# Optimization experiments

Measured on AMD Instinct MI355X. Metric: run time of the kernel, lower is better.

## Reference

```python
import jax, jax.numpy as jnp
import numpy as np

N = 8192
HID = 256
NCLS = 5
K = 10  # adj_parameter
IN_DIMS = [1000, 1000, 503]


def _leaky(x):
    return jnp.where(x >= 0, x, 0.25 * x)


def _batchnorm(x, g, b):
    # training-mode BatchNorm1d with batch stats (biased var), eps=1e-5
    mu = jnp.mean(x, axis=0)
    var = jnp.mean((x - mu) ** 2, axis=0)
    return (x - mu) * jax.lax.rsqrt(var + 1e-5) * g + b


def _build_adj(feat):
    # cosine similarity, per-row top-(K+1) (top-1 is self, diag=1), scatter,
    # add identity, L1 row-normalize. Vectorized equivalent of the torch loop.
    norm = jnp.maximum(jnp.linalg.norm(feat, axis=1, keepdims=True), 1e-12)
    fn = feat / norm
    sim = fn @ fn.T                                  # [N, N]
    vals, idx = jax.lax.top_k(sim, K + 1)            # [N, K+1]
    rows = jnp.arange(sim.shape[0])[:, None]
    adj = jnp.zeros_like(sim).at[rows, idx[:, 1:]].set(vals[:, 1:])
    adj = adj + jnp.eye(sim.shape[0], dtype=sim.dtype)
    rs = jnp.maximum(jnp.sum(jnp.abs(adj), axis=1, keepdims=True), 1e-12)
    return adj / rs


def setup_inputs() -> dict:
    key = jax.random.key(0)
    ks = jax.random.split(key, 24)
    d = {}
    d['x1'] = jax.random.normal(ks[0], (N, IN_DIMS[0]), jnp.float32)
    d['x2'] = jax.random.normal(ks[1], (N, IN_DIMS[1]), jnp.float32)
    d['x3'] = jax.random.normal(ks[2], (N, IN_DIMS[2]), jnp.float32)
    def xavier(k, shape):
        fan_in, fan_out = shape[-2], shape[-1]
        std = np.sqrt(2.0 / (fan_in + fan_out))
        return jax.random.normal(k, shape, jnp.float32) * std
    d['enc_W1'] = xavier(ks[3], (IN_DIMS[0], HID))
    d['enc_W2'] = xavier(ks[4], (IN_DIMS[1], HID))
    d['enc_W3'] = xavier(ks[5], (IN_DIMS[2], HID))
    d['enc_b'] = jnp.zeros((3, HID), jnp.float32)
    d['bn_g'] = jnp.ones((3, HID), jnp.float32)
    d['bn_b'] = jnp.zeros((3, HID), jnp.float32)
    d['gc1_W'] = xavier(ks[6], (3, HID, HID))
    d['gc1_b'] = jnp.zeros((3, HID), jnp.float32)
    d['gc2_W'] = xavier(ks[7], (3, HID, HID))
    d['gc2_b'] = jnp.zeros((3, HID), jnp.float32)
    d['clf_W'] = xavier(ks[8], (3, HID, NCLS))
    d['clf_b'] = jnp.zeros((3, NCLS), jnp.float32)
    d['attn'] = xavier(ks[9], (3, 1))[:, 0]
    d['f1_W'] = xavier(ks[10], (NCLS, 128))
    d['f1_b'] = jnp.zeros((128,), jnp.float32)
    d['f2_W'] = xavier(ks[11], (128, NCLS))
    d['f2_b'] = jnp.zeros((NCLS,), jnp.float32)
    return d


def reference(x1, x2, x3, enc_W1, enc_W2, enc_W3, enc_b, bn_g, bn_b,
              gc1_W, gc1_b, gc2_W, gc2_b, clf_W, clf_b,
              attn, f1_W, f1_b, f2_W, f2_b):
    xs = [x1, x2, x3]
    enc_Ws = [enc_W1, enc_W2, enc_W3]
    logits_list = []
    for i in range(3):
        # modal encoder: Linear -> ReLU -> BatchNorm (dropout off, eval)
        feat = jax.nn.relu(xs[i] @ enc_Ws[i] + enc_b[i])
        feat = _batchnorm(feat, bn_g[i], bn_b[i])
        adj = _build_adj(feat)
        # SimpleGCN: two GraphConvolution layers with leaky_relu(0.25)
        h = _leaky(adj @ (feat @ gc1_W[i]) + gc1_b[i])
        h = _leaky(adj @ (h @ gc2_W[i]) + gc2_b[i])
        logits_list.append(h @ clf_W[i] + clf_b[i])
    # SimpleVCDN fusion
    w = jax.nn.softmax(attn)
    fused = sum(w[i] * jax.nn.sigmoid(logits_list[i]) for i in range(3))
    out = _leaky(fused @ f1_W + f1_b) @ f2_W + f2_b
    return out
```

## Files before the change

### kernel.cpp

```cpp
#include <hip/hip_runtime.h>
#include <cfloat>
#include <cstdint>
#include <cstddef>

#define NROWS 8192
#define HID 256
#define NCLS 5
#define TOPK 10
#define CAP 256
#define TM 128
#define TN 128
#define BK 32
#define BKS 64

typedef __bf16 bf16x8 __attribute__((ext_vector_type(8)));
typedef float f32x4 __attribute__((ext_vector_type(4)));

__device__ inline ushort f2bf(float x) {
  unsigned u = __float_as_uint(x);
  unsigned r = (u + 0x7fffu + ((u >> 16) & 1u)) >> 16;
  return (ushort)r;
}
__device__ inline float bf2f(ushort b) { return __uint_as_float(((unsigned)b) << 16); }

__device__ __forceinline__ void load_lds16(const void* g, void* l) {
  __builtin_amdgcn_global_load_lds(
      (const __attribute__((address_space(1))) void*)g,
      (__attribute__((address_space(3))) void*)l, 16, 0, 0);
}

__global__ __launch_bounds__(256) void packAB_kernel(const float* __restrict__ X0,
    const float* __restrict__ X1, const float* __restrict__ X2,
    const float* __restrict__ W0, const float* __restrict__ W1,
    const float* __restrict__ W2, ushort* __restrict__ Ah, ushort* __restrict__ Al,
    ushort* __restrict__ Bh, ushort* __restrict__ Bl,
    int D0, int D1, int D2, int Kp0, int Kp1, int Kp2,
    size_t aOff0, size_t aOff1, size_t aOff2,
    size_t wOff0, size_t wOff1, size_t wOff2) {
  const int z = blockIdx.y;
  const float* X = (z == 0) ? X0 : (z == 1) ? X1 : X2;
  const float* W = (z == 0) ? W0 : (z == 1) ? W1 : W2;
  const int D = (z == 0) ? D0 : (z == 1) ? D1 : D2;
  const int Kp = (z == 0) ? Kp0 : (z == 1) ? Kp1 : Kp2;
  const size_t aOff = (z == 0) ? aOff0 : (z == 1) ? aOff1 : aOff2;
  const size_t wOff = (z == 0) ? wOff0 : (z == 1) ? wOff1 : wOff2;
  const int ksh = 31 - __clz(Kp);
  const int id = blockIdx.x * 256 + threadIdx.x;
  const int atotal = NROWS << ksh;
  if (id >= atotal + (HID << ksh)) return;
  if (id < atotal) {
    const int k = id & (Kp - 1);
    const int r = id >> ksh;
    const float x = (k < D) ? X[(size_t)r * D + k] : 0.f;
    const ushort h = f2bf(x);
    Ah[aOff + id] = h;
    Al[aOff + id] = f2bf(x - bf2f(h));
  } else {
    const int id2 = id - atotal;
    const int k = id2 & (Kp - 1);
    const int n = id2 >> ksh;
    const float x = (k < D) ? W[(size_t)k * HID + n] : 0.f;
    const ushort h = f2bf(x);
    Bh[wOff + id2] = h;
    Bl[wOff + id2] = f2bf(x - bf2f(h));
  }
}

__global__ __launch_bounds__(256) void packW_kernel(const float* __restrict__ W,
    ushort* __restrict__ Bh, ushort* __restrict__ Bl) {
  const int z = blockIdx.y;
  const int id = blockIdx.x * 256 + threadIdx.x;
  const int k = id >> 8, n = id & 255;
  const size_t wz = (size_t)z * HID * HID;
  const float x = W[wz + (size_t)k * HID + n];
  const ushort h = f2bf(x);
  Bh[wz + (size_t)n * HID + k] = h;
  Bl[wz + (size_t)n * HID + k] = f2bf(x - bf2f(h));
}

template<bool BIAS, int ACT>
__global__ __launch_bounds__(256) void limbgemm_kernel(const ushort* __restrict__ Ah,
    const ushort* __restrict__ Al, const ushort* __restrict__ Bh,
    const ushort* __restrict__ Bl, const float* __restrict__ bias,
    float* __restrict__ C, int Kp0, int Kp1, int Kp2,
    size_t aOff0, size_t aOff1, size_t aOff2,
    size_t bOff0, size_t bOff1, size_t bOff2) {
  __shared__ ushort AsH[64 * BK], AsL[64 * BK], BsH[64 * BK], BsL[64 * BK];
  const int z = blockIdx.y;
  const int Kp = (z == 0) ? Kp0 : (z == 1) ? Kp1 : Kp2;
  const size_t aO = (z == 0) ? aOff0 : (z == 1) ? aOff1 : aOff2;
  const size_t bO = (z == 0) ? bOff0 : (z == 1) ? bOff1 : bOff2;
  Ah += aO; Al += aO; Bh += bO; Bl += bO;
  C += (size_t)z * NROWS * HID;
  const int tid = threadIdx.x;
  const int wave = tid >> 6, lane = tid & 63;
  const int bid = blockIdx.x;
  const int xcd = bid & 7, slot = bid >> 3;
  const int bxi = slot & 3;
  const int byi = xcd * 16 + (slot >> 2);
  const int bm = byi * 64, bn = bxi * 64;
  const int wr = (wave >> 1) * 32, wc = (wave & 1) * 32;

  f32x4 acc[2][2];
  const f32x4 zero = {0.f, 0.f, 0.f, 0.f};
  acc[0][0] = zero; acc[0][1] = zero; acc[1][0] = zero; acc[1][1] = zero;

  const int r0 = tid >> 2, kl0 = (tid & 3) ^ ((r0 & 3) ^ ((r0 >> 2) & 1));
  const size_t aoff = (size_t)(bm + r0) * Kp + kl0 * 8;
  const size_t boff = (size_t)(bn + r0) * Kp + kl0 * 8;

  for (int k0 = 0; k0 < Kp; k0 += BK) {
    __syncthreads();
    load_lds16(Ah + aoff + k0, &AsH[tid * 8]);
    load_lds16(Al + aoff + k0, &AsL[tid * 8]);
    load_lds16(Bh + boff + k0, &BsH[tid * 8]);
    load_lds16(Bl + boff + k0, &BsL[tid * 8]);
    __syncthreads();
    bf16x8 ah[2], al[2], bh[2], bl[2];
    const int kg = lane >> 4;
    #pragma unroll
    for (int f = 0; f < 2; ++f) {
      const int m = wr + f * 16 + (lane & 15);
      const int sa = m * 4 + (kg ^ (m & 3) ^ ((m >> 2) & 1));
      ah[f] = *(const bf16x8*)&AsH[sa * 8];
      al[f] = *(const bf16x8*)&AsL[sa * 8];
      const int n = wc + f * 16 + (lane & 15);
      const int sb = n * 4 + (kg ^ (n & 3) ^ ((n >> 2) & 1));
      bh[f] = *(const bf16x8*)&BsH[sb * 8];
      bl[f] = *(const bf16x8*)&BsL[sb * 8];
    }
    #pragma unroll
    for (int fr = 0; fr < 2; ++fr)
      #pragma unroll
      for (int fc = 0; fc < 2; ++fc) {
        acc[fr][fc] = __builtin_amdgcn_mfma_f32_16x16x32_bf16(ah[fr], bh[fc], acc[fr][fc], 0, 0, 0);
        acc[fr][fc] = __builtin_amdgcn_mfma_f32_16x16x32_bf16(ah[fr], bl[fc], acc[fr][fc], 0, 0, 0);
        acc[fr][fc] = __builtin_amdgcn_mfma_f32_16x16x32_bf16(al[fr], bh[fc], acc[fr][fc], 0, 0, 0);
      }
  }
  const int cq = lane >> 4, cc = lane & 15;
  #pragma unroll
  for (int fr = 0; fr < 2; ++fr) {
    #pragma unroll
    for (int fc = 0; fc < 2; ++fc) {
      const int rb = bm + wr + fr * 16 + cq * 4;
      const int col = bn + wc + fc * 16 + cc;
      const float bb = BIAS ? bias[z * HID + col] : 0.f;
      float* cp = C + (size_t)rb * HID + col;
      #pragma unroll
      for (int e = 0; e < 4; ++e) {
        float v = acc[fr][fc][e] + bb;
        if (ACT == 1) v = fmaxf(v, 0.f);
        cp[(size_t)e * HID] = v;
      }
    }
  }
}

__global__ __launch_bounds__(256) void bn_stats_kernel(const float* __restrict__ F,
    float* __restrict__ ps, float* __restrict__ ps2) {
  const int z = blockIdx.y;
  const int b = blockIdx.x, t = threadIdx.x;
  float s = 0.f, s2 = 0.f;
  const float* p = F + (size_t)z * NROWS * HID + (size_t)b * 128 * HID + t;
  for (int r = 0; r < 128; ++r) {
    const float v = p[(size_t)r * HID];
    s += v; s2 += v * v;
  }
  ps[(size_t)z * 64 * HID + b * HID + t] = s;
  ps2[(size_t)z * 64 * HID + b * HID + t] = s2;
}

__global__ __launch_bounds__(256) void bn_finalize_kernel(const float* __restrict__ ps,
    const float* __restrict__ ps2, const float* __restrict__ g,
    const float* __restrict__ b, float* __restrict__ scale, float* __restrict__ shift) {
  const int z = blockIdx.x;
  const int t = threadIdx.x;
  float s = 0.f, s2 = 0.f;
  for (int i = 0; i < 64; ++i) {
    s += ps[(size_t)z * 64 * HID + i * HID + t];
    s2 += ps2[(size_t)z * 64 * HID + i * HID + t];
  }
  const float mu = s / (float)NROWS;
  const float var = s2 / (float)NROWS - mu * mu;
  const float rstd = rsqrtf(var + 1e-5f);
  const float sc = rstd * g[z * HID + t];
  scale[z * HID + t] = sc;
  shift[z * HID + t] = b[z * HID + t] - mu * sc;
}

__global__ __launch_bounds__(256) void bn_rownorm_kernel(const float* __restrict__ F,
    const float* __restrict__ scale, const float* __restrict__ shift,
    float* __restrict__ FN, ushort* __restrict__ Ph,
    ushort* __restrict__ Fh, ushort* __restrict__ Fl) {
  const int z = blockIdx.y;
  const int r = blockIdx.x, t = threadIdx.x;
  const size_t zb = (size_t)z * NROWS * HID;
  const float f = F[zb + (size_t)r * HID + t] * scale[z * HID + t] + shift[z * HID + t];
  __shared__ float sh[256];
  sh[t] = f * f;
  __syncthreads();
  for (int st = 128; st > 0; st >>= 1) {
    if (t < st) sh[t] += sh[t + st];
    __syncthreads();
  }
  const float inv = 1.0f / fmaxf(sqrtf(sh[0]), 1e-12f);
  const float fn = f * inv;
  const size_t o = zb + (size_t)r * HID + t;
  FN[o] = fn;
  Ph[o] = f2bf(fn);
  const ushort h = f2bf(f);
  Fh[o] = h;
  Fl[o] = f2bf(f - bf2f(h));
}

template<int PASS>
__global__ __launch_bounds__(512) void simtile_kernel(const ushort* __restrict__ P,
    float* __restrict__ M, const float* __restrict__ tauv,
    int* __restrict__ gcnt, int* __restrict__ gidx) {
  const int bx = blockIdx.x, by = blockIdx.y;
  if (by > bx) return;
  const int z = blockIdx.z;
  P += (size_t)z * NROWS * HID;
  if (PASS == 0) M += (size_t)z * NROWS * 64;
  else {
    tauv += (size_t)z * NROWS;
    gcnt += (size_t)z * NROWS;
    gidx += (size_t)z * NROWS * CAP;
  }
  const bool offdiag = (bx != by);
  __shared__ ushort As[TM * BKS];
  __shared__ ushort Bs[TN * BKS];
  __shared__ float Ml[2][TM];
  __shared__ float MlC[4][TN];
  __shared__ float taulA[TM];
  __shared__ float taulB[TN];
  const int tid = threadIdx.x;
  const int wave = tid >> 6, lane = tid & 63;
  const int bm = by * TM;
  const int bn = bx * TN;
  const int wr = (wave >> 1) * 32;
  const int wc = (wave & 1) * 64;

  if (PASS == 1) {
    if (tid < TM) taulA[tid] = tauv[bm + tid];
    else if (tid < TM + TN) taulB[tid - TM] = tauv[bn + (tid - TM)];
  }

  const ushort* pa[2];
  const ushort* pb[2];
  #pragma unroll
  for (int j = 0; j < 2; ++j) {
    const int s = tid + j * 512;
    const int m = s >> 3;
    const int kg = (s & 7) ^ (m & 7);
    pa[j] = P + (size_t)(bm + m) * HID + kg * 8;
    pb[j] = P + (size_t)(bn + m) * HID + kg * 8;
  }

  f32x4 acc[2][4];
  const f32x4 zero = {0.f, 0.f, 0.f, 0.f};
  #pragma unroll
  for (int i = 0; i < 2; ++i)
    #pragma unroll
    for (int j = 0; j < 4; ++j) acc[i][j] = zero;

  for (int k0 = 0; k0 < HID; k0 += BKS) {
    __syncthreads();
    #pragma unroll
    for (int j = 0; j < 2; ++j) {
      load_lds16(pa[j] + k0, &As[(tid + j * 512) * 8]);
      load_lds16(pb[j] + k0, &Bs[(tid + j * 512) * 8]);
    }
    __syncthreads();
    #pragma unroll
    for (int h = 0; h < 2; ++h) {
      const int kgb = h * 4 + (lane >> 4);
      bf16x8 af[2], bf[4];
      #pragma unroll
      for (int f = 0; f < 2; ++f) {
        const int m = wr + f * 16 + (lane & 15);
        const int sa = m * 8 + (kgb ^ (m & 7));
        af[f] = *(const bf16x8*)&As[sa * 8];
      }
      #pragma unroll
      for (int f = 0; f < 4; ++f) {
        const int n = wc + f * 16 + (lane & 15);
        const int sb = n * 8 + (kgb ^ (n & 7));
        bf[f] = *(const bf16x8*)&Bs[sb * 8];
      }
      #pragma unroll
      for (int fr = 0; fr < 2; ++fr)
        #pragma unroll
        for (int fc = 0; fc < 4; ++fc)
          acc[fr][fc] = __builtin_amdgcn_mfma_f32_16x16x32_bf16(af[fr], bf[fc], acc[fr][fc], 0, 0, 0);
    }
  }

  const int cq = lane >> 4, cc = lane & 15;
  if (PASS == 0) {
    #pragma unroll
    for (int fr = 0; fr < 2; ++fr) {
      #pragma unroll
      for (int e = 0; e < 4; ++e) {
        const int lrow = wr + fr * 16 + cq * 4 + e;
        const int grow = bm + lrow;
        float mx = -FLT_MAX;
        #pragma unroll
        for (int fc = 0; fc < 4; ++fc) {
          const int col = bn + wc + fc * 16 + cc;
          mx = fmaxf(mx, (col == grow) ? -FLT_MAX : acc[fr][fc][e]);
        }
        #pragma unroll
        for (int s = 1; s < 16; s <<= 1) mx = fmaxf(mx, __shfl_xor(mx, s));
        if (cc == 0) Ml[wave & 1][lrow] = mx;
      }
    }
    if (offdiag) {
      #pragma unroll
      for (int fc = 0; fc < 4; ++fc) {
        float mx = -FLT_MAX;
        #pragma unroll
        for (int fr = 0; fr < 2; ++fr)
          #pragma unroll
          for (int e = 0; e < 4; ++e) mx = fmaxf(mx, acc[fr][fc][e]);
        mx = fmaxf(mx, __shfl_xor(mx, 16));
        mx = fmaxf(mx, __shfl_xor(mx, 32));
        if (cq == 0) MlC[wave >> 1][wc + fc * 16 + cc] = mx;
      }
    }
    __syncthreads();
    if (tid < TM) M[(size_t)(bm + tid) * 64 + bx] = fmaxf(Ml[0][tid], Ml[1][tid]);
    if (offdiag && tid < TN) {
      const float mx = fmaxf(fmaxf(MlC[0][tid], MlC[1][tid]),
                             fmaxf(MlC[2][tid], MlC[3][tid]));
      M[(size_t)(bn + tid) * 64 + by] = mx;
    }
  } else {
    __syncthreads();
    #pragma unroll
    for (int fr = 0; fr < 2; ++fr) {
      #pragma unroll
      for (int e = 0; e < 4; ++e) {
        const int lrow = wr + fr * 16 + cq * 4 + e;
        const int grow = bm + lrow;
        const float tA = taulA[lrow];
        #pragma unroll
        for (int fc = 0; fc < 4; ++fc) {
          const int lcol = wc + fc * 16 + cc;
          const int gcol = bn + lcol;
          const float v = acc[fr][fc][e];
          if (gcol != grow && v >= tA) {
            const int pos = atomicAdd(&gcnt[grow], 1);
            if (pos < CAP) gidx[(size_t)grow * CAP + pos] = gcol;
          }
          if (offdiag && v >= taulB[lcol]) {
            const int pos = atomicAdd(&gcnt[gcol], 1);
            if (pos < CAP) gidx[(size_t)gcol * CAP + pos] = grow;
          }
        }
      }
    }
  }
}

__global__ __launch_bounds__(256) void tau_kernel(const float* __restrict__ M,
    float* __restrict__ tauv, int* __restrict__ gcnt) {
  const int z = blockIdx.y;
  const int wave = threadIdx.x >> 6, lane = threadIdx.x & 63;
  const int row = blockIdx.x * 4 + wave;
  float cur = M[(size_t)z * NROWS * 64 + (size_t)row * 64 + lane];
  float tau = cur;
  #pragma unroll
  for (int sel = 0; sel < 16; ++sel) {
    float bv = cur;
    int bl = lane;
    #pragma unroll
    for (int s = 1; s < 64; s <<= 1) {
      const float ov = __shfl_xor(bv, s);
      const int ol = __shfl_xor(bl, s);
      if (ov > bv || (ov == bv && ol < bl)) { bv = ov; bl = ol; }
    }
    tau = bv;
    if (lane == bl) cur = -FLT_MAX;
  }
  if (lane == 0) {
    tauv[(size_t)z * NROWS + row] = tau;
    gcnt[(size_t)z * NROWS + row] = 0;
  }
}

__global__ __launch_bounds__(256) void refine_kernel(const int* __restrict__ gcnt,
    const int* __restrict__ gidx, const float* __restrict__ FN,
    int* __restrict__ nidx, float* __restrict__ nval, float* __restrict__ dinv) {
  const int z = blockIdx.y;
  gcnt += (size_t)z * NROWS;
  gidx += (size_t)z * NROWS * CAP;
  FN += (size_t)z * NROWS * HID;
  nidx += (size_t)z * NROWS * TOPK;
  nval += (size_t)z * NROWS * TOPK;
  dinv += (size_t)z * NROWS;
  const int wave = threadIdx.x >> 6, lane = threadIdx.x & 63;
  const int row = blockIdx.x * 4 + wave;
  const int cnt = min(gcnt[row], CAP);
  __shared__ float fnrow[4][HID];
  __shared__ float ev[4][CAP];
  ((float4*)fnrow[wave])[lane] = ((const float4*)(FN + (size_t)row * HID))[lane];
  __syncthreads();
  const int c = lane >> 2, q4 = lane & 3;
  for (int b0 = 0; b0 < cnt; b0 += 16) {
    const int ci = b0 + c;
    const int cand = (ci < cnt) ? gidx[(size_t)row * CAP + ci] : 0;
    float s = 0.f;
    const float* fc = FN + (size_t)cand * HID + q4 * 64;
    const float* fr = fnrow[wave] + q4 * 64;
    #pragma unroll 8
    for (int k = 0; k < 64; ++k) s += fr[k] * fc[k];
    s += __shfl_xor(s, 1);
    s += __shfl_xor(s, 2);
    if (q4 == 0 && ci < cnt) ev[wave][ci] = s;
  }
  __syncthreads();
  float outv[TOPK];
  int outi[TOPK];
  float sum = 1.0f;
  #pragma unroll
  for (int sel = 0; sel < TOPK; ++sel) {
    float bv = -FLT_MAX;
    int bp = 0;
    #pragma unroll
    for (int j = 0; j < 4; ++j) {
      const int p = lane + j * 64;
      if (p < cnt) {
        const float v = ev[wave][p];
        if (v > bv) { bv = v; bp = p; }
      }
    }
    #pragma unroll
    for (int s = 1; s < 64; s <<= 1) {
      const float ov = __shfl_xor(bv, s);
      const int op = __shfl_xor(bp, s);
      if (ov > bv || (ov == bv && op < bp)) { bv = ov; bp = op; }
    }
    outv[sel] = bv;
    outi[sel] = bp;
    sum += fabsf(bv);
    if (lane == 0) ev[wave][bp] = -FLT_MAX;
  }
  if (lane == 0) {
    const float inv = 1.0f / fmaxf(sum, 1e-12f);
    dinv[row] = inv;
    #pragma unroll
    for (int sel = 0; sel < TOPK; ++sel) {
      nval[row * TOPK + sel] = outv[sel] * inv;
      nidx[row * TOPK + sel] = gidx[(size_t)row * CAP + outi[sel]];
    }
  }
}

template<int EMIT>
__global__ __launch_bounds__(256) void spmm_kernel(const float* __restrict__ T,
    const int* __restrict__ nidx, const float* __restrict__ nval,
    const float* __restrict__ dinv, const float* __restrict__ bias,
    float* __restrict__ H, ushort* __restrict__ Hh, ushort* __restrict__ Hl) {
  const int z = blockIdx.y;
  const size_t zb = (size_t)z * NROWS * HID;
  T += zb;
  nidx += (size_t)z * NROWS * TOPK;
  nval += (size_t)z * NROWS * TOPK;
  dinv += (size_t)z * NROWS;
  const int r = blockIdx.x, c = threadIdx.x;
  float acc = dinv[r] * T[(size_t)r * HID + c];
  #pragma unroll
  for (int n = 0; n < TOPK; ++n) {
    acc += nval[r * TOPK + n] * T[(size_t)nidx[r * TOPK + n] * HID + c];
  }
  acc += bias[z * HID + c];
  const float v = acc >= 0.f ? acc : 0.25f * acc;
  const size_t o = zb + (size_t)r * HID + c;
  if (EMIT == 0) {
    H[o] = v;
  } else {
    const ushort h = f2bf(v);
    Hh[o] = h;
    Hl[o] = f2bf(v - bf2f(h));
  }
}

__global__ __launch_bounds__(256) void clf_kernel(const float* __restrict__ H,
    const float* __restrict__ W, const float* __restrict__ b,
    float* __restrict__ L) {
  const int z = blockIdx.y;
  const int id = blockIdx.x * 256 + threadIdx.x;
  if (id >= NROWS * NCLS) return;
  const int r = id / NCLS, c = id % NCLS;
  float s = b[z * NCLS + c];
  const float* hr = H + (size_t)z * NROWS * HID + (size_t)r * HID;
  const float* wz = W + (size_t)z * HID * NCLS;
  for (int k = 0; k < HID; ++k) s += hr[k] * wz[k * NCLS + c];
  L[(size_t)z * NROWS * NCLS + id] = s;
}

__global__ __launch_bounds__(256) void fuse_kernel(const float* __restrict__ L,
    const float* __restrict__ attn, float* __restrict__ fused) {
  const int id = blockIdx.x * 256 + threadIdx.x;
  if (id >= NROWS * NCLS) return;
  const float a0 = attn[0], a1 = attn[1], a2 = attn[2];
  const float m = fmaxf(a0, fmaxf(a1, a2));
  const float e0 = expf(a0 - m), e1 = expf(a1 - m), e2 = expf(a2 - m);
  const float inv = 1.0f / (e0 + e1 + e2);
  const float l0 = L[id];
  const float l1 = L[NROWS * NCLS + id];
  const float l2 = L[2 * NROWS * NCLS + id];
  const float s0 = 1.0f / (1.0f + expf(-l0));
  const float s1 = 1.0f / (1.0f + expf(-l1));
  const float s2 = 1.0f / (1.0f + expf(-l2));
  fused[id] = (e0 * s0 + e1 * s1 + e2 * s2) * inv;
}

__global__ __launch_bounds__(128) void head_kernel(const float* __restrict__ fused,
    const float* __restrict__ W1, const float* __restrict__ b1,
    const float* __restrict__ W2, const float* __restrict__ b2,
    float* __restrict__ out) {
  const int r = blockIdx.x, t = threadIdx.x;
  __shared__ float f[NCLS];
  __shared__ float hh[128];
  if (t < NCLS) f[t] = fused[r * NCLS + t];
  __syncthreads();
  float s = b1[t];
  #pragma unroll
  for (int k = 0; k < NCLS; ++k) s += f[k] * W1[k * 128 + t];
  hh[t] = s >= 0.f ? s : 0.25f * s;
  __syncthreads();
  if (t < NCLS) {
    float o = b2[t];
    for (int k = 0; k < 128; ++k) o += hh[k] * W2[k * NCLS + t];
    out[r * NCLS + t] = o;
  }
}

extern "C" void kernel_launch(void* const* d_in, const int* in_sizes, int n_in,
                              void* d_out, int out_size, void* d_ws, size_t ws_size,
                              hipStream_t stream) {
  const float* x0 = (const float*)d_in[0];
  const float* x1 = (const float*)d_in[1];
  const float* x2 = (const float*)d_in[2];
  const float* eW0 = (const float*)d_in[3];
  const float* eW1 = (const float*)d_in[4];
  const float* eW2 = (const float*)d_in[5];
  const float* enc_b = (const float*)d_in[6];
  const float* bn_g  = (const float*)d_in[7];
  const float* bn_b  = (const float*)d_in[8];
  const float* gc1W  = (const float*)d_in[9];
  const float* gc1b  = (const float*)d_in[10];
  const float* gc2W  = (const float*)d_in[11];
  const float* gc2b  = (const float*)d_in[12];
  const float* clfW  = (const float*)d_in[13];
  const float* clfb  = (const float*)d_in[14];
  const float* attn  = (const float*)d_in[15];
  const float* f1W   = (const float*)d_in[16];
  const float* f1b   = (const float*)d_in[17];
  const float* f2W   = (const float*)d_in[18];
  const float* f2b   = (const float*)d_in[19];
  float* out = (float*)d_out;

  int Kp[3];
  for (int m = 0; m < 3; ++m) {
    const int D = in_sizes[m] / NROWS;
    int k = 256;
    while (k < D) k <<= 1;
    Kp[m] = k;
  }
  const size_t KpSum = (size_t)Kp[0] + Kp[1] + Kp[2];
  const int D0 = in_sizes[0] / NROWS, D1 = in_sizes[1] / NROWS, D2 = in_sizes[2] / NROWS;

  const size_t NH = (size_t)NROWS * HID;
  float* ws = (float*)d_ws;
  float* A = ws;
  float* C = A;
  float* nval = A + 3 * NH;
  int*   nidx = (int*)(nval + (size_t)3 * NROWS * TOPK);
  float* dinv = (float*)(nidx + (size_t)3 * NROWS * TOPK);
  float* logits = dinv + 3 * NROWS;
  float* fused = logits + (size_t)3 * NROWS * NCLS;
  float* ps    = fused + (size_t)NROWS * NCLS;
  float* ps2   = ps + 3 * 64 * HID;
  float* scale = ps2 + 3 * 64 * HID;
  float* shift = scale + 3 * HID;
  float* M     = shift + 3 * HID;
  float* tauv  = M + (size_t)3 * NROWS * 64;
  int*   gcnt  = (int*)(tauv + 3 * NROWS);
  int*   gidx  = gcnt + 3 * NROWS;
  float* Bf    = (float*)gidx;
  ushort* WhG = (ushort*)(gidx + (size_t)3 * NROWS * CAP);
  ushort* WlG = WhG + (size_t)3 * HID * HID;
  ushort* WhE = WlG + (size_t)3 * HID * HID;
  ushort* WlE = WhE + (size_t)HID * KpSum;
  char* u3 = (char*)(WlE + (size_t)HID * KpSum);
  float* FN = (float*)u3;
  ushort* Ph = (ushort*)(FN + 3 * NH);
  ushort* Fh = Ph + 3 * NH;
  ushort* Fl = Fh + 3 * NH;
  ushort* Hh = Fl + 3 * NH;
  ushort* Hl = Hh + 3 * NH;
  ushort* AhE = (ushort*)u3;
  ushort* AlE = AhE + (size_t)NROWS * KpSum;

  const size_t aOff0 = 0, aOff1 = (size_t)NROWS * Kp[0],
               aOff2 = (size_t)NROWS * (Kp[0] + Kp[1]);
  const size_t wOff0 = 0, wOff1 = (size_t)HID * Kp[0],
               wOff2 = (size_t)HID * (Kp[0] + Kp[1]);

  const dim3 blk(256);
  packAB_kernel<<<dim3(((NROWS + HID) * 1024) / 256, 3), blk, 0, stream>>>(
      x0, x1, x2, eW0, eW1, eW2, AhE, AlE, WhE, WlE,
      D0, D1, D2, Kp[0], Kp[1], Kp[2], aOff0, aOff1, aOff2, wOff0, wOff1, wOff2);
  limbgemm_kernel<true, 1><<<dim3(512, 3), blk, 0, stream>>>(
      AhE, AlE, WhE, WlE, enc_b, A, Kp[0], Kp[1], Kp[2],
      aOff0, aOff1, aOff2, wOff0, wOff1, wOff2);
  bn_stats_kernel<<<dim3(64, 3), blk, 0, stream>>>(A, ps, ps2);
  bn_finalize_kernel<<<3, blk, 0, stream>>>(ps, ps2, bn_g, bn_b, scale, shift);
  bn_rownorm_kernel<<<dim3(NROWS, 3), blk, 0, stream>>>(A, scale, shift, FN, Ph, Fh, Fl);
  simtile_kernel<0><<<dim3(64, 64, 3), dim3(512), 0, stream>>>(Ph, M, nullptr, nullptr, nullptr);
  tau_kernel<<<dim3(NROWS / 4, 3), blk, 0, stream>>>(M, tauv, gcnt);
  simtile_kernel<1><<<dim3(64, 64, 3), dim3(512), 0, stream>>>(Ph, nullptr, tauv, gcnt, gidx);
  refine_kernel<<<dim3(NROWS / 4, 3), blk, 0, stream>>>(gcnt, gidx, FN, nidx, nval, dinv);
  packW_kernel<<<dim3(256, 3), blk, 0, stream>>>(gc1W, WhG, WlG);
  limbgemm_kernel<false, 0><<<dim3(512, 3), blk, 0, stream>>>(
      Fh, Fl, WhG, WlG, nullptr, C, HID, HID, HID,
      0, NH, 2 * NH, 0, (size_t)HID * HID, (size_t)2 * HID * HID);
  spmm_kernel<1><<<dim3(NROWS, 3), blk, 0, stream>>>(C, nidx, nval, dinv, gc1b,
                                                     nullptr, Hh, Hl);
  packW_kernel<<<dim3(256, 3), blk, 0, stream>>>(gc2W, WhG, WlG);
  limbgemm_kernel<false, 0><<<dim3(512, 3), blk, 0, stream>>>(
      Hh, Hl, WhG, WlG, nullptr, C, HID, HID, HID,
      0, NH, 2 * NH, 0, (size_t)HID * HID, (size_t)2 * HID * HID);
  spmm_kernel<0><<<dim3(NROWS, 3), blk, 0, stream>>>(C, nidx, nval, dinv, gc2b,
                                                     Bf, nullptr, nullptr);
  clf_kernel<<<dim3((NROWS * NCLS + 255) / 256, 3), blk, 0, stream>>>(Bf, clfW, clfb, logits);
  fuse_kernel<<<(NROWS * NCLS + 255) / 256, blk, 0, stream>>>(logits, attn, fused);
  head_kernel<<<NROWS, dim3(128), 0, stream>>>(fused, f1W, f1b, f2W, f2b, out);
}
```

Before: 839.0 us.

## Enlarge limb GEMM tiles to 128x128 and fuse classifier into second SpMM

The split-bf16 limb GEMM moves from 64x64 block tiles with 2x2 MFMA fragments per wave to 128x128 tiles with 4x4 fragments per wave, launching a quarter as many blocks. This raises operand reuse from LDS and cuts global traffic per output. Separately, the second SpMM now computes the 5-class classifier directly through wave shuffle reductions, removing the fp32 hidden-state write and the separate classifier kernel. In exchange, the GEMM uses more accumulator registers and LDS and has fewer blocks to fill the GPU.

```diff
diff --git a/kernel.cpp b/kernel.cpp
--- a/kernel.cpp
+++ b/kernel.cpp
@@ -85,7 +85,7 @@
     float* __restrict__ C, int Kp0, int Kp1, int Kp2,
     size_t aOff0, size_t aOff1, size_t aOff2,
     size_t bOff0, size_t bOff1, size_t bOff2) {
-  __shared__ ushort AsH[64 * BK], AsL[64 * BK], BsH[64 * BK], BsL[64 * BK];
+  __shared__ ushort AsH[TM * BK], AsL[TM * BK], BsH[TM * BK], BsL[TM * BK];
   const int z = blockIdx.y;
   const int Kp = (z == 0) ? Kp0 : (z == 1) ? Kp1 : Kp2;
   const size_t aO = (z == 0) ? aOff0 : (z == 1) ? aOff1 : aOff2;
@@ -96,30 +96,41 @@
   const int wave = tid >> 6, lane = tid & 63;
   const int bid = blockIdx.x;
   const int xcd = bid & 7, slot = bid >> 3;
-  const int bxi = slot & 3;
-  const int byi = xcd * 16 + (slot >> 2);
-  const int bm = byi * 64, bn = bxi * 64;
-  const int wr = (wave >> 1) * 32, wc = (wave & 1) * 32;
-
-  f32x4 acc[2][2];
+  const int bxi = slot & 1;
+  const int byi = xcd * 8 + (slot >> 1);
+  const int bm = byi * TM, bn = bxi * 128;
+  const int wr = (wave >> 1) * 64, wc = (wave & 1) * 64;
+
+  f32x4 acc[4][4];
   const f32x4 zero = {0.f, 0.f, 0.f, 0.f};
-  acc[0][0] = zero; acc[0][1] = zero; acc[1][0] = zero; acc[1][1] = zero;
-
-  const int r0 = tid >> 2, kl0 = (tid & 3) ^ ((r0 & 3) ^ ((r0 >> 2) & 1));
-  const size_t aoff = (size_t)(bm + r0) * Kp + kl0 * 8;
-  const size_t boff = (size_t)(bn + r0) * Kp + kl0 * 8;
+  #pragma unroll
+  for (int i = 0; i < 4; ++i)
+    #pragma unroll
+    for (int j = 0; j < 4; ++j) acc[i][j] = zero;
+
+  const int p0 = tid, p1 = tid + 256;
+  const int r0 = p0 >> 2, kl0 = (p0 & 3) ^ ((r0 & 3) ^ ((r0 >> 2) & 1));
+  const int r1 = p1 >> 2, kl1 = (p1 & 3) ^ ((r1 & 3) ^ ((r1 >> 2) & 1));
+  const size_t a0 = (size_t)(bm + r0) * Kp + kl0 * 8;
+  const size_t a1 = (size_t)(bm + r1) * Kp + kl1 * 8;
+  const size_t b0 = (size_t)(bn + r0) * Kp + kl0 * 8;
+  const size_t b1 = (size_t)(bn + r1) * Kp + kl1 * 8;
 
   for (int k0 = 0; k0 < Kp; k0 += BK) {
     __syncthreads();
-    load_lds16(Ah + aoff + k0, &AsH[tid * 8]);
-    load_lds16(Al + aoff + k0, &AsL[tid * 8]);
-    load_lds16(Bh + boff + k0, &BsH[tid * 8]);
-    load_lds16(Bl + boff + k0, &BsL[tid * 8]);
-    __syncthreads();
-    bf16x8 ah[2], al[2], bh[2], bl[2];
+    load_lds16(Ah + a0 + k0, &AsH[p0 * 8]);
+    load_lds16(Ah + a1 + k0, &AsH[p1 * 8]);
+    load_lds16(Al + a0 + k0, &AsL[p0 * 8]);
+    load_lds16(Al + a1 + k0, &AsL[p1 * 8]);
+    load_lds16(Bh + b0 + k0, &BsH[p0 * 8]);
+    load_lds16(Bh + b1 + k0, &BsH[p1 * 8]);
+    load_lds16(Bl + b0 + k0, &BsL[p0 * 8]);
+    load_lds16(Bl + b1 + k0, &BsL[p1 * 8]);
+    __syncthreads();
+    bf16x8 ah[4], al[4], bh[4], bl[4];
     const int kg = lane >> 4;
     #pragma unroll
-    for (int f = 0; f < 2; ++f) {
+    for (int f = 0; f < 4; ++f) {
       const int m = wr + f * 16 + (lane & 15);
       const int sa = m * 4 + (kg ^ (m & 3) ^ ((m >> 2) & 1));
       ah[f] = *(const bf16x8*)&AsH[sa * 8];
@@ -130,9 +141,9 @@
       bl[f] = *(const bf16x8*)&BsL[sb * 8];
     }
     #pragma unroll
-    for (int fr = 0; fr < 2; ++fr)
-      #pragma unroll
-      for (int fc = 0; fc < 2; ++fc) {
+    for (int fr = 0; fr < 4; ++fr)
+      #pragma unroll
+      for (int fc = 0; fc < 4; ++fc) {
         acc[fr][fc] = __builtin_amdgcn_mfma_f32_16x16x32_bf16(ah[fr], bh[fc], acc[fr][fc], 0, 0, 0);
         acc[fr][fc] = __builtin_amdgcn_mfma_f32_16x16x32_bf16(ah[fr], bl[fc], acc[fr][fc], 0, 0, 0);
         acc[fr][fc] = __builtin_amdgcn_mfma_f32_16x16x32_bf16(al[fr], bh[fc], acc[fr][fc], 0, 0, 0);
@@ -140,9 +151,9 @@
   }
   const int cq = lane >> 4, cc = lane & 15;
   #pragma unroll
-  for (int fr = 0; fr < 2; ++fr) {
-    #pragma unroll
-    for (int fc = 0; fc < 2; ++fc) {
+  for (int fr = 0; fr < 4; ++fr) {
+    #pragma unroll
+    for (int fc = 0; fc < 4; ++fc) {
       const int rb = bm + wr + fr * 16 + cq * 4;
       const int col = bn + wc + fc * 16 + cc;
       const float bb = BIAS ? bias[z * HID + col] : 0.f;
@@ -462,7 +473,9 @@
 __global__ __launch_bounds__(256) void spmm_kernel(const float* __restrict__ T,
     const int* __restrict__ nidx, const float* __restrict__ nval,
     const float* __restrict__ dinv, const float* __restrict__ bias,
-    float* __restrict__ H, ushort* __restrict__ Hh, ushort* __restrict__ Hl) {
+    ushort* __restrict__ Hh, ushort* __restrict__ Hl,
+    const float* __restrict__ clfW, const float* __restrict__ clfb,
+    float* __restrict__ L) {
   const int z = blockIdx.y;
   const size_t zb = (size_t)z * NROWS * HID;
   T += zb;
@@ -477,28 +490,28 @@
   }
   acc += bias[z * HID + c];
   const float v = acc >= 0.f ? acc : 0.25f * acc;
-  const size_t o = zb + (size_t)r * HID + c;
-  if (EMIT == 0) {
-    H[o] = v;
-  } else {
+  if (EMIT == 1) {
+    const size_t o = zb + (size_t)r * HID + c;
     const ushort h = f2bf(v);
     Hh[o] = h;
     Hl[o] = f2bf(v - bf2f(h));
-  }
-}
-
-__global__ __launch_bounds__(256) void clf_kernel(const float* __restrict__ H,
-    const float* __restrict__ W, const float* __restrict__ b,
-    float* __restrict__ L) {
-  const int z = blockIdx.y;
-  const int id = blockIdx.x * 256 + threadIdx.x;
-  if (id >= NROWS * NCLS) return;
-  const int r = id / NCLS, c = id % NCLS;
-  float s = b[z * NCLS + c];
-  const float* hr = H + (size_t)z * NROWS * HID + (size_t)r * HID;
-  const float* wz = W + (size_t)z * HID * NCLS;
-  for (int k = 0; k < HID; ++k) s += hr[k] * wz[k * NCLS + c];
-  L[(size_t)z * NROWS * NCLS + id] = s;
+  } else {
+    __shared__ float wsum[4][NCLS];
+    const int wave = c >> 6, lane = c & 63;
+    const float* wrow = clfW + (size_t)z * HID * NCLS + (size_t)c * NCLS;
+    #pragma unroll
+    for (int cls = 0; cls < NCLS; ++cls) {
+      float p = v * wrow[cls];
+      #pragma unroll
+      for (int s = 1; s < 64; s <<= 1) p += __shfl_xor(p, s);
+      if (lane == 0) wsum[wave][cls] = p;
+    }
+    __syncthreads();
+    if (c < NCLS) {
+      const float lg = clfb[z * NCLS + c] + wsum[0][c] + wsum[1][c] + wsum[2][c] + wsum[3][c];
+      L[(size_t)z * NROWS * NCLS + (size_t)r * NCLS + c] = lg;
+    }
+  }
 }
 
 __global__ __launch_bounds__(256) void fuse_kernel(const float* __restrict__ L,
@@ -591,7 +604,6 @@
   float* tauv  = M + (size_t)3 * NROWS * 64;
   int*   gcnt  = (int*)(tauv + 3 * NROWS);
   int*   gidx  = gcnt + 3 * NROWS;
-  float* Bf    = (float*)gidx;
   ushort* WhG = (ushort*)(gidx + (size_t)3 * NROWS * CAP);
   ushort* WlG = WhG + (size_t)3 * HID * HID;
   ushort* WhE = WlG + (size_t)3 * HID * HID;
@@ -615,7 +627,7 @@
   packAB_kernel<<<dim3(((NROWS + HID) * 1024) / 256, 3), blk, 0, stream>>>(
       x0, x1, x2, eW0, eW1, eW2, AhE, AlE, WhE, WlE,
       D0, D1, D2, Kp[0], Kp[1], Kp[2], aOff0, aOff1, aOff2, wOff0, wOff1, wOff2);
-  limbgemm_kernel<true, 1><<<dim3(512, 3), blk, 0, stream>>>(
+  limbgemm_kernel<true, 1><<<dim3(128, 3), blk, 0, stream>>>(
       AhE, AlE, WhE, WlE, enc_b, A, Kp[0], Kp[1], Kp[2],
       aOff0, aOff1, aOff2, wOff0, wOff1, wOff2);
   bn_stats_kernel<<<dim3(64, 3), blk, 0, stream>>>(A, ps, ps2);
@@ -626,18 +638,17 @@
   simtile_kernel<1><<<dim3(64, 64, 3), dim3(512), 0, stream>>>(Ph, nullptr, tauv, gcnt, gidx);
   refine_kernel<<<dim3(NROWS / 4, 3), blk, 0, stream>>>(gcnt, gidx, FN, nidx, nval, dinv);
   packW_kernel<<<dim3(256, 3), blk, 0, stream>>>(gc1W, WhG, WlG);
-  limbgemm_kernel<false, 0><<<dim3(512, 3), blk, 0, stream>>>(
+  limbgemm_kernel<false, 0><<<dim3(128, 3), blk, 0, stream>>>(
       Fh, Fl, WhG, WlG, nullptr, C, HID, HID, HID,
       0, NH, 2 * NH, 0, (size_t)HID * HID, (size_t)2 * HID * HID);
   spmm_kernel<1><<<dim3(NROWS, 3), blk, 0, stream>>>(C, nidx, nval, dinv, gc1b,
-                                                     nullptr, Hh, Hl);
+                                                     Hh, Hl, nullptr, nullptr, nullptr);
   packW_kernel<<<dim3(256, 3), blk, 0, stream>>>(gc2W, WhG, WlG);
-  limbgemm_kernel<false, 0><<<dim3(512, 3), blk, 0, stream>>>(
+  limbgemm_kernel<false, 0><<<dim3(128, 3), blk, 0, stream>>>(
       Hh, Hl, WhG, WlG, nullptr, C, HID, HID, HID,
       0, NH, 2 * NH, 0, (size_t)HID * HID, (size_t)2 * HID * HID);
   spmm_kernel<0><<<dim3(NROWS, 3), blk, 0, stream>>>(C, nidx, nval, dinv, gc2b,
-                                                     Bf, nullptr, nullptr);
-  clf_kernel<<<dim3((NROWS * NCLS + 255) / 256, 3), blk, 0, stream>>>(Bf, clfW, clfb, logits);
+                                                     nullptr, nullptr, clfW, clfb, logits);
   fuse_kernel<<<(NROWS * NCLS + 255) / 256, blk, 0, stream>>>(logits, attn, fused);
   head_kernel<<<NROWS, dim3(128), 0, stream>>>(fused, f1W, f1b, f2W, f2b, out);
 }
```

New measurement: 810.2 us. 1.04x faster.
